# Kernel tuning notes

Hardware: AMD Instinct MI355X
Metric: run time of the kernel (lower is better)

## Reference

```python
import jax, jax.numpy as jnp
import numpy as np

N = 200000      # num nodes
D = 64          # n_dims_in == n_dims_out
Q = 4096        # num queries
G = 64          # edges per query in last step (contiguous groups, G > max_edges)
E = Q * G       # last-step edges
E0 = 131072     # earlier-step edges
K = 10          # max_edges (top-k per query)
RATIO = 0.0     # ratio_update


def setup_inputs() -> dict:
    key = jax.random.key(0)
    ks = jax.random.split(key, 14)
    # last-step edges: [E,8]; col0=query id (sorted, contiguous groups of G), col6=src, col7=dst
    q1 = jnp.repeat(jnp.arange(Q, dtype=jnp.int32), G)
    src1 = jax.random.randint(ks[0], (E,), 0, N, dtype=jnp.int32)
    dst1 = jax.random.randint(ks[1], (E,), 0, N, dtype=jnp.int32)
    edges1 = jnp.concatenate([q1[:, None], jnp.zeros((E, 5), jnp.int32), src1[:, None], dst1[:, None]], axis=1)
    # earlier-step edges: [E0,8]
    q0 = jax.random.randint(ks[2], (E0,), 0, Q, dtype=jnp.int32)
    src0 = jax.random.randint(ks[3], (E0,), 0, N, dtype=jnp.int32)
    dst0 = jax.random.randint(ks[4], (E0,), 0, N, dtype=jnp.int32)
    edges0 = jnp.concatenate([q0[:, None], jnp.zeros((E0, 5), jnp.int32), src0[:, None], dst0[:, None]], axis=1)
    std_g3 = np.float32(np.sqrt(2.0 / (4 * D)))
    std_x = np.float32(np.sqrt(2.0 / (D + D)))  # xavier_normal for linear_between_steps
    return {
        "visited_node_score": jax.random.uniform(ks[5], (N,), dtype=jnp.float32),
        "node_repr": jax.random.normal(ks[6], (N, D), dtype=jnp.float32),
        "rel_emb0": jax.random.normal(ks[7], (E0, D), dtype=jnp.float32),
        "rel_emb1": jax.random.normal(ks[8], (E, D), dtype=jnp.float32),
        "rule_prior": jax.random.normal(ks[9], (E,), dtype=jnp.float32),
        "query_src_ts_emb": jax.random.normal(ks[10], (Q, D), dtype=jnp.float32),
        "query_rel_emb": jax.random.normal(ks[11], (Q, D), dtype=jnp.float32),
        "Wq": jax.random.normal(ks[12], (4 * D, 4 * D), dtype=jnp.float32) * std_g3,
        "Wk": jax.random.normal(ks[13], (4 * D, 4 * D), dtype=jnp.float32) * std_g3,
        "W_lin": jax.random.normal(jax.random.fold_in(key, 77), (D, D), dtype=jnp.float32) * std_x,
        "b_lin": jnp.zeros((D,), dtype=jnp.float32),
        "rule_gamma": jnp.float32(1.0),
        "edges0": edges0,
        "edges1": edges1,
        "max_edges": K,
    }


def _segment_softmax(logits, seg, n):
    m = jax.ops.segment_max(logits, seg, num_segments=n)
    e = jnp.exp(logits - m[seg])
    s = jax.ops.segment_sum(e, seg, num_segments=n)
    return e / s[seg]


def _att_score(q_idx, h_vi, h_vj, rel, qst_tab, qr_tab, Wq, Wk):
    qst = qst_tab[q_idx]
    qr = qr_tab[q_idx]
    left = jnp.concatenate([h_vi, rel, qst, qr], axis=-1)   # [E, 4D]
    right = jnp.concatenate([h_vj, rel, qst, qr], axis=-1)  # [E, 4D]
    return jnp.sum((left @ Wq.T) * (right @ Wk.T), axis=-1)  # [E]


def _update_repr(src, dst, repr_, trans, n):
    # sparse mm: row src <- (1-ratio)*trans * repr[dst]; diag = 1 for non-src nodes, ratio for src nodes
    agg = jax.ops.segment_sum(trans[:, None] * repr_[dst], src, num_segments=n)
    has_src = jax.ops.segment_sum(jnp.ones_like(trans), src, num_segments=n) > 0
    diag = jnp.where(has_src, jnp.float32(RATIO), jnp.float32(1.0))
    return (1.0 - RATIO) * agg + diag[:, None] * repr_


def reference(visited_node_score, node_repr, rel_emb0, rel_emb1, rule_prior,
              query_src_ts_emb, query_rel_emb, Wq, Wk, W_lin, b_lin, rule_gamma,
              edges0, edges1, max_edges):
    n = node_repr.shape[0]
    qid, src, dst = edges1[:, 0], edges1[:, 6], edges1[:, 7]
    # last propagation step: rule-aware attention
    logits = _att_score(qid, node_repr[src], node_repr[dst], rel_emb1,
                        query_src_ts_emb, query_rel_emb, Wq, Wk) + rule_gamma * rule_prior
    src_score = visited_node_score[src]
    trans = _segment_softmax(logits, src, n)
    target_score = trans * src_score
    # per-query top-k (groups are contiguous blocks of size G, all > k)
    ts2 = target_score.reshape(-1, G)                                 # [Q, G]
    _, idx = jax.lax.top_k(ts2, max_edges)                            # [Q, k]
    orig_indices = (jnp.arange(ts2.shape[0], dtype=idx.dtype)[:, None] * G + idx).reshape(-1)
    pruned_edges = edges1[orig_indices]
    trans_p = trans[orig_indices]
    pruned_src_score = src_score[orig_indices]
    # node score update: sparse [n, Ep] @ src_score == scatter-add by target node (col 7)
    updated_node_score = jax.ops.segment_sum(trans_p * pruned_src_score, pruned_edges[:, 7], num_segments=n)
    updated_repr = _update_repr(pruned_edges[:, 6], pruned_edges[:, 7], node_repr, trans_p, n)
    # earlier step (back-propagation of representations)
    s0, d0 = edges0[:, 6], edges0[:, 7]
    l0 = _att_score(edges0[:, 0], updated_repr[s0], updated_repr[d0], rel_emb0,
                    query_src_ts_emb, query_rel_emb, Wq, Wk)
    t0 = _segment_softmax(l0, s0, n)
    updated_repr = _update_repr(s0, d0, updated_repr, t0, n)
    # bypass_forward: LeakyReLU(Linear(.))
    updated_repr = jax.nn.leaky_relu(updated_repr @ W_lin.T + b_lin, negative_slope=0.01)
    return updated_node_score, updated_repr, pruned_edges, orig_indices
```

## Files before the change

### kernel.cpp

```cpp
#include <hip/hip_runtime.h>

#define NN 200000
#define QQ 4096
#define GG 64
#define EE 262144
#define EE0 131072
#define KK 10
#define QKp (QQ*KK)

#define o_M      0
#define o_GpT    16384
#define o_P      65536
#define o_sQ     1114112
#define o_segmax 1118208
#define o_segsum 1318208
#define o_has    1518208
#define o_elog   1718208
#define o_rm22   1980352
#define o_target 2242496
#define o_psrc   2504640
#define o_pdst   2545600
#define o_pt     2586560
#define o_g      2627520
#define o_end    (o_g+12800000)

__device__ __forceinline__ float dot4(float4 a, float4 b){
  return a.x*b.x + a.y*b.y + a.z*b.z + a.w*b.w;
}
__device__ __forceinline__ unsigned fenc(float f){
  unsigned u = __float_as_uint(f);
  return (u & 0x80000000u) ? ~u : (u | 0x80000000u);
}
__device__ __forceinline__ float fdec(unsigned e){
  return (e & 0x80000000u) ? __uint_as_float(e ^ 0x80000000u) : __uint_as_float(~e);
}

__global__ void computeG_k(const float* __restrict__ Wq, const float* __restrict__ Wk,
                           float* __restrict__ G){
  __shared__ float wa[64][64], wb[64][64];
  int m = blockIdx.x;
  int aoff = (m>>2)*64, boff = (m&3)*64;
  int t = threadIdx.x;
  int j = t & 63, g = t >> 6;
  float acc[16];
  #pragma unroll
  for (int ii=0; ii<16; ii++) acc[ii]=0.f;
  for (int k0=0; k0<256; k0+=64){
    for (int s=0; s<16; s++){
      int kk = g*16 + s;
      wa[kk][j] = Wq[(k0+kk)*256 + aoff + j];
      wb[kk][j] = Wk[(k0+kk)*256 + boff + j];
    }
    __syncthreads();
    for (int kk=0; kk<64; kk++){
      float bv = wb[kk][j];
      #pragma unroll
      for (int ii=0; ii<16; ii++) acc[ii] += wa[kk][g*16+ii]*bv;
    }
    __syncthreads();
  }
  for (int ii=0; ii<16; ii++) G[(aoff + g*16+ii)*256 + boff + j] = acc[ii];
}

__global__ void repack_k(const float* __restrict__ G, float* __restrict__ M,
                         float* __restrict__ GpT){
  int t = blockIdx.x*256 + threadIdx.x;
  if (t < 16384){
    int m = t >> 12, r = (t >> 6) & 63, c = t & 63;
    float v;
    if (m==0)      v = G[r*256 + c];
    else if (m==1) v = G[(64+r)*256 + c];
    else if (m==2) v = G[c*256 + 64 + r];
    else           v = G[(64+r)*256 + 64 + c];
    M[t] = v;
  } else {
    int u = t - 16384;
    int j = u / 384, i = u - j*384;
    GpT[u] = (i < 128) ? G[i*256 + 128 + j] : G[(128+j)*256 + (i-128)];
  }
}

__global__ void pq_k(const float* __restrict__ QST, const float* __restrict__ QR,
                     const float* __restrict__ GpT, float* __restrict__ P,
                     float* __restrict__ sQ){
  __shared__ float xs[4][128];
  int wv = threadIdx.x >> 6, lane = threadIdx.x & 63;
  int q = blockIdx.x*4 + wv;
  xs[wv][lane]      = QST[(size_t)q*64 + lane];
  xs[wv][64 + lane] = QR[(size_t)q*64 + lane];
  __syncthreads();
  float4 accP = {0.f,0.f,0.f,0.f};
  float4 accY = {0.f,0.f,0.f,0.f};
  for (int j=0; j<128; j++){
    float xv = xs[wv][j];
    float4 gpv = ((const float4*)(GpT + j*384))[lane];
    accP.x += gpv.x*xv; accP.y += gpv.y*xv; accP.z += gpv.z*xv; accP.w += gpv.w*xv;
    if (lane < 32){
      float4 gyv = ((const float4*)(GpT + j*384 + 256))[lane];
      accY.x += gyv.x*xv; accY.y += gyv.y*xv; accY.z += gyv.z*xv; accY.w += gyv.w*xv;
    }
  }
  ((float4*)(P + (size_t)q*256))[lane] = accP;
  float sq = 0.f;
  if (lane < 32){
    sq = accY.x*xs[wv][4*lane] + accY.y*xs[wv][4*lane+1]
       + accY.z*xs[wv][4*lane+2] + accY.w*xs[wv][4*lane+3];
  }
  #pragma unroll
  for (int off=32; off>0; off>>=1) sq += __shfl_xor(sq, off, 64);
  if (lane == 0) sQ[q] = sq;
}

__global__ void matvec64_k(const float* __restrict__ X, const float* __restrict__ W,
                           float* __restrict__ O, int rows){
  int r = blockIdx.x*blockDim.x + threadIdx.x;
  if (r >= rows) return;
  const float4* Xv = (const float4*)(X + (size_t)r*64);
  float4 x[16];
  #pragma unroll
  for (int jj=0;jj<16;jj++) x[jj] = Xv[jj];
  const float4* Wv = (const float4*)W;
  float4* Ov = (float4*)(O + (size_t)r*64);
  for (int i0=0; i0<16; i0++){
    float a[4];
    #pragma unroll
    for (int ii=0; ii<4; ii++){
      float s=0.f;
      #pragma unroll
      for (int jj=0;jj<16;jj++) s += dot4(Wv[(i0*4+ii)*16+jj], x[jj]);
      a[ii]=s;
    }
    Ov[i0] = make_float4(a[0],a[1],a[2],a[3]);
  }
}

__global__ void quadform_k(const float* __restrict__ X, const float* __restrict__ W,
                           float* __restrict__ O, int rows){
  int r = blockIdx.x*blockDim.x + threadIdx.x;
  if (r >= rows) return;
  const float4* Xv = (const float4*)(X + (size_t)r*64);
  float4 x[16];
  #pragma unroll
  for (int jj=0;jj<16;jj++) x[jj] = Xv[jj];
  const float4* Wv = (const float4*)W;
  float acc = 0.f;
  #pragma unroll
  for (int i0=0; i0<16; i0++){
    float xi[4] = {x[i0].x, x[i0].y, x[i0].z, x[i0].w};
    #pragma unroll
    for (int ii=0; ii<4; ii++){
      float s=0.f;
      #pragma unroll
      for (int jj=0;jj<16;jj++) s += dot4(Wv[(i0*4+ii)*16+jj], x[jj]);
      acc += xi[ii]*s;
    }
  }
  O[r] = acc;
}

__global__ void linear_leaky_k(const float* __restrict__ X, const float* __restrict__ W,
                               const float* __restrict__ bias, float* __restrict__ O, int rows){
  int r = blockIdx.x*blockDim.x + threadIdx.x;
  if (r >= rows) return;
  const float4* Xv = (const float4*)(X + (size_t)r*64);
  float4 x[16];
  #pragma unroll
  for (int jj=0;jj<16;jj++) x[jj] = Xv[jj];
  const float4* Wv = (const float4*)W;
  float4* Ov = (float4*)(O + (size_t)r*64);
  for (int i0=0; i0<16; i0++){
    float a[4];
    #pragma unroll
    for (int ii=0; ii<4; ii++){
      float s = bias[i0*4+ii];
      #pragma unroll
      for (int jj=0;jj<16;jj++) s += dot4(Wv[(i0*4+ii)*16+jj], x[jj]);
      a[ii] = (s >= 0.f) ? s : 0.01f*s;
    }
    Ov[i0] = make_float4(a[0],a[1],a[2],a[3]);
  }
}

__global__ void passQ_k(const int* __restrict__ edges, const float* __restrict__ H,
                        const float* __restrict__ REL, const float* __restrict__ P,
                        const float* __restrict__ sQ, const float* __restrict__ rm22,
                        const float* __restrict__ prior, const float* __restrict__ gamma_p,
                        float* __restrict__ logits, int nE){
  int w = (blockIdx.x*blockDim.x + threadIdx.x) >> 6;
  int lane = threadIdx.x & 63;
  if (w >= nE) return;
  int q = edges[(size_t)w*8 + 0];
  int s = edges[(size_t)w*8 + 6];
  int d = edges[(size_t)w*8 + 7];
  const float* Pq = P + (size_t)q*256;
  float hs = H[(size_t)s*64 + lane];
  float hd = H[(size_t)d*64 + lane];
  float rr = REL[(size_t)w*64 + lane];
  float acc = hs*Pq[lane] + hd*Pq[128+lane] + rr*(Pq[64+lane]+Pq[192+lane]);
  #pragma unroll
  for (int off=32; off>0; off>>=1) acc += __shfl_xor(acc, off, 64);
  if (lane == 0){
    float lg = acc + sQ[q] + rm22[w];
    if (prior) lg += gamma_p[0]*prior[w];
    logits[w] = lg;
  }
}

__global__ void dot_k(const int* __restrict__ edges, const float* __restrict__ H,
                      const float* __restrict__ REL, const float* __restrict__ g,
                      float* __restrict__ logits, unsigned* __restrict__ segmax,
                      int mode, int nE){
  int w = (blockIdx.x*blockDim.x + threadIdx.x) >> 6;
  int lane = threadIdx.x & 63;
  if (w >= nE) return;
  int s = edges[(size_t)w*8 + 6];
  int d = edges[(size_t)w*8 + 7];
  float a, b;
  if (mode == 0){ a = H[(size_t)s*64 + lane];   b = g[(size_t)d*64 + lane]; }
  else if (mode == 1){ a = REL[(size_t)w*64 + lane]; b = g[(size_t)d*64 + lane]; }
  else { a = REL[(size_t)w*64 + lane]; b = g[(size_t)s*64 + lane]; }
  float acc = a*b;
  #pragma unroll
  for (int off=32; off>0; off>>=1) acc += __shfl_xor(acc, off, 64);
  if (lane == 0){
    float lg = logits[w] + acc;
    logits[w] = lg;
    if (mode == 2) atomicMax(&segmax[s], fenc(lg));
  }
}

__global__ void expsum_k(const int* __restrict__ edges, float* __restrict__ elog,
                         const unsigned* __restrict__ segmax,
                         float* __restrict__ segsum, int* __restrict__ has, int nE){
  int e = blockIdx.x*blockDim.x + threadIdx.x;
  if (e >= nE) return;
  int s = edges[(size_t)e*8 + 6];
  float m = fdec(segmax[s]);
  float ev = expf(elog[e] - m);
  elog[e] = ev;
  atomicAdd(&segsum[s], ev);
  if (has) has[s] = 1;
}

__global__ void trans_k(const int* __restrict__ edges, float* __restrict__ elog,
                        const float* __restrict__ segsum, const float* __restrict__ vscore,
                        float* __restrict__ target, int nE){
  int e = blockIdx.x*blockDim.x + threadIdx.x;
  if (e >= nE) return;
  int s = edges[(size_t)e*8 + 6];
  float t = elog[e] / segsum[s];
  elog[e] = t;
  if (target) target[e] = t * vscore[s];
}

__global__ void topk_k(const float* __restrict__ target, const float* __restrict__ trans,
                       const int* __restrict__ edges, const float* __restrict__ vscore,
                       float* __restrict__ out_score, float* __restrict__ out_pruned,
                       float* __restrict__ out_orig, int* __restrict__ psrc, int* __restrict__ pdst,
                       float* __restrict__ pt, int* __restrict__ has){
  int q = blockIdx.x*4 + (threadIdx.x>>6);
  int lane = threadIdx.x & 63;
  if (q >= QQ) return;
  float myv = target[(size_t)q*GG + lane];
  for (int j=0;j<KK;j++){
    float v = myv; int idx = lane;
    #pragma unroll
    for (int off=32; off>0; off>>=1){
      float ov = __shfl_xor(v, off, 64);
      int oi = __shfl_xor(idx, off, 64);
      if (ov > v || (ov == v && oi < idx)){ v = ov; idx = oi; }
    }
    if (lane == idx){
      myv = -__builtin_inff();
      int orig = q*GG + idx;
      out_orig[q*KK + j] = (float)orig;
      int s = edges[(size_t)orig*8 + 6];
      int d = edges[(size_t)orig*8 + 7];
      #pragma unroll
      for (int c=0;c<8;c++) out_pruned[((size_t)q*KK+j)*8 + c] = (float)edges[(size_t)orig*8 + c];
      float t = trans[orig];
      float ss = vscore[s];
      atomicAdd(&out_score[d], t*ss);
      psrc[q*KK+j] = s; pdst[q*KK+j] = d; pt[q*KK+j] = t;
      has[s] = 1;
    }
  }
}

__global__ void scatter_pruned_k(const int* __restrict__ psrc, const int* __restrict__ pdst,
                                 const float* __restrict__ pt, const float* __restrict__ H,
                                 float* __restrict__ agg){
  int p = (blockIdx.x*blockDim.x + threadIdx.x) >> 6;
  int lane = threadIdx.x & 63;
  if (p >= QKp) return;
  int s = psrc[p], d = pdst[p];
  float t = pt[p];
  atomicAdd(&agg[(size_t)s*64 + lane], t * H[(size_t)d*64 + lane]);
}

__global__ void scatter_edges_k(const int* __restrict__ edges, const float* __restrict__ trans,
                                const float* __restrict__ H, float* __restrict__ agg, int nE){
  int e = (blockIdx.x*blockDim.x + threadIdx.x) >> 6;
  int lane = threadIdx.x & 63;
  if (e >= nE) return;
  int s = edges[(size_t)e*8 + 6];
  int d = edges[(size_t)e*8 + 7];
  atomicAdd(&agg[(size_t)s*64 + lane], trans[e] * H[(size_t)d*64 + lane]);
}

__global__ void fixup_copy_k(const int* __restrict__ has, const float* __restrict__ src,
                             float* __restrict__ dstbuf){
  int i = blockIdx.x*blockDim.x + threadIdx.x;
  if (i >= NN*64) return;
  int v = i >> 6;
  if (!has[v]) dstbuf[i] = src[i];
}

extern "C" void kernel_launch(void* const* d_in, const int* in_sizes, int n_in,
                              void* d_out, int out_size, void* d_ws, size_t ws_size,
                              hipStream_t stream){
  const float* vscore    = (const float*)d_in[0];
  const float* node_repr = (const float*)d_in[1];
  const float* rel0      = (const float*)d_in[2];
  const float* rel1      = (const float*)d_in[3];
  const float* prior     = (const float*)d_in[4];
  const float* qst       = (const float*)d_in[5];
  const float* qre       = (const float*)d_in[6];
  const float* Wq        = (const float*)d_in[7];
  const float* Wk        = (const float*)d_in[8];
  const float* Wlin      = (const float*)d_in[9];
  const float* blin      = (const float*)d_in[10];
  const float* gamma     = (const float*)d_in[11];
  const int*   edges0    = (const int*)d_in[12];
  const int*   edges1    = (const int*)d_in[13];

  float* ws = (float*)d_ws;
  float* M      = ws + o_M;
  float* GpT    = ws + o_GpT;
  float* P      = ws + o_P;
  float* sQv    = ws + o_sQ;
  unsigned* segmax = (unsigned*)(ws + o_segmax);
  float* segsum = ws + o_segsum;
  int*   has    = (int*)(ws + o_has);
  float* elog   = ws + o_elog;
  float* rm22   = ws + o_rm22;
  float* target = ws + o_target;
  int*   psrc   = (int*)(ws + o_psrc);
  int*   pdst   = (int*)(ws + o_pdst);
  float* pt     = ws + o_pt;
  float* gbuf   = ws + o_g;

  float* out_score  = (float*)d_out;
  float* out_repr   = out_score + NN;
  float* out_pruned = out_repr + (size_t)NN*64;
  float* out_orig   = out_pruned + (size_t)QKp*8;

  const float* M00  = M + 0;
  const float* M10  = M + 4096;
  const float* M01T = M + 8192;
  const float* M11b = M + 12288;

  hipMemsetAsync(ws + o_segmax, 0, (size_t)600000*4, stream);
  hipMemsetAsync(out_score, 0, (size_t)(NN + (size_t)NN*64)*4, stream);

  computeG_k<<<16,256,0,stream>>>(Wq, Wk, gbuf);
  repack_k<<<256,256,0,stream>>>(gbuf, M, GpT);
  pq_k<<<QQ/4,256,0,stream>>>(qst, qre, GpT, P, sQv);

  quadform_k<<<EE/256,256,0,stream>>>(rel1, M11b, rm22, EE);
  passQ_k<<<EE/4,256,0,stream>>>(edges1, node_repr, rel1, P, sQv, rm22,
                                 prior, gamma, elog, EE);
  matvec64_k<<<(NN+255)/256,256,0,stream>>>(node_repr, M00, gbuf, NN);
  dot_k<<<EE/4,256,0,stream>>>(edges1, node_repr, rel1, gbuf, elog, segmax, 0, EE);
  matvec64_k<<<(NN+255)/256,256,0,stream>>>(node_repr, M10, gbuf, NN);
  dot_k<<<EE/4,256,0,stream>>>(edges1, node_repr, rel1, gbuf, elog, segmax, 1, EE);
  matvec64_k<<<(NN+255)/256,256,0,stream>>>(node_repr, M01T, gbuf, NN);
  dot_k<<<EE/4,256,0,stream>>>(edges1, node_repr, rel1, gbuf, elog, segmax, 2, EE);
  expsum_k<<<EE/256,256,0,stream>>>(edges1, elog, segmax, segsum, nullptr, EE);
  trans_k<<<EE/256,256,0,stream>>>(edges1, elog, segsum, vscore, target, EE);
  topk_k<<<QQ/4,256,0,stream>>>(target, elog, edges1, vscore, out_score, out_pruned, out_orig,
                                psrc, pdst, pt, has);
  scatter_pruned_k<<<(QKp*64)/256,256,0,stream>>>(psrc, pdst, pt, node_repr, out_repr);
  fixup_copy_k<<<(NN*64+255)/256,256,0,stream>>>(has, node_repr, out_repr);

  hipMemsetAsync(ws + o_segmax, 0, (size_t)600000*4, stream);
  quadform_k<<<EE0/256,256,0,stream>>>(rel0, M11b, rm22, EE0);
  passQ_k<<<EE0/4,256,0,stream>>>(edges0, out_repr, rel0, P, sQv, rm22,
                                  nullptr, nullptr, elog, EE0);
  matvec64_k<<<(NN+255)/256,256,0,stream>>>(out_repr, M00, gbuf, NN);
  dot_k<<<EE0/4,256,0,stream>>>(edges0, out_repr, rel0, gbuf, elog, segmax, 0, EE0);
  matvec64_k<<<(NN+255)/256,256,0,stream>>>(out_repr, M10, gbuf, NN);
  dot_k<<<EE0/4,256,0,stream>>>(edges0, out_repr, rel0, gbuf, elog, segmax, 1, EE0);
  matvec64_k<<<(NN+255)/256,256,0,stream>>>(out_repr, M01T, gbuf, NN);
  dot_k<<<EE0/4,256,0,stream>>>(edges0, out_repr, rel0, gbuf, elog, segmax, 2, EE0);
  expsum_k<<<EE0/256,256,0,stream>>>(edges0, elog, segmax, segsum, has, EE0);
  trans_k<<<EE0/256,256,0,stream>>>(edges0, elog, segsum, vscore, nullptr, EE0);
  hipMemsetAsync(gbuf, 0, (size_t)NN*64*4, stream);
  scatter_edges_k<<<(EE0*64)/256,256,0,stream>>>(edges0, elog, out_repr, gbuf, EE0);
  fixup_copy_k<<<(NN*64+255)/256,256,0,stream>>>(has, out_repr, gbuf);
  linear_leaky_k<<<(NN+255)/256,256,0,stream>>>(gbuf, Wlin, blin, out_repr, NN);
}
```

Baseline: 1.413 ms.

## Stage row tiles through LDS for coalesced matvec I/O and fuse init with fixup copy

The per-row matvec, quadform and linear_leaky kernels now stage 64-row tiles through padded LDS, so global loads and stores are coalesced float4 accesses instead of each thread streaming its own 256-byte row. They run as 64-thread blocks. The large memset plus fixup copy around each scatter is replaced by one init kernel that writes zeros for rows with incoming edges and copies the source for the rest, saving a full pass over the N×64 buffer. Small blocks may lower occupancy, and the launches now assume row counts divisible by 64.

```diff
diff --git a/kernel.cpp b/kernel.cpp
--- a/kernel.cpp
+++ b/kernel.cpp
@@ -7,6 +7,7 @@
 #define EE0 131072
 #define KK 10
 #define QKp (QQ*KK)
+#define PITCH 68
 
 #define o_M      0
 #define o_GpT    16384
@@ -111,16 +112,25 @@
   if (lane == 0) sQ[q] = sq;
 }
 
-__global__ void matvec64_k(const float* __restrict__ X, const float* __restrict__ W,
-                           float* __restrict__ O, int rows){
-  int r = blockIdx.x*blockDim.x + threadIdx.x;
-  if (r >= rows) return;
-  const float4* Xv = (const float4*)(X + (size_t)r*64);
+__global__ __launch_bounds__(64) void matvec64_k(const float* __restrict__ X,
+                                                 const float* __restrict__ W,
+                                                 float* __restrict__ O){
+  __shared__ float lds[64*PITCH];
+  int lane = threadIdx.x;
+  size_t base = (size_t)blockIdx.x * 64;
+  const float4* Xg = (const float4*)(X + base*64);
+  #pragma unroll
+  for (int i=0;i<16;i++){
+    int f = i*64 + lane;
+    float4 v = Xg[f];
+    *(float4*)(lds + (f>>4)*PITCH + (f&15)*4) = v;
+  }
+  __builtin_amdgcn_sched_barrier(0);
   float4 x[16];
   #pragma unroll
-  for (int jj=0;jj<16;jj++) x[jj] = Xv[jj];
+  for (int jj=0;jj<16;jj++) x[jj] = *(const float4*)(lds + lane*PITCH + jj*4);
+  __builtin_amdgcn_sched_barrier(0);
   const float4* Wv = (const float4*)W;
-  float4* Ov = (float4*)(O + (size_t)r*64);
   for (int i0=0; i0<16; i0++){
     float a[4];
     #pragma unroll
@@ -130,18 +140,34 @@
       for (int jj=0;jj<16;jj++) s += dot4(Wv[(i0*4+ii)*16+jj], x[jj]);
       a[ii]=s;
     }
-    Ov[i0] = make_float4(a[0],a[1],a[2],a[3]);
-  }
-}
-
-__global__ void quadform_k(const float* __restrict__ X, const float* __restrict__ W,
-                           float* __restrict__ O, int rows){
-  int r = blockIdx.x*blockDim.x + threadIdx.x;
-  if (r >= rows) return;
-  const float4* Xv = (const float4*)(X + (size_t)r*64);
+    *(float4*)(lds + lane*PITCH + i0*4) = make_float4(a[0],a[1],a[2],a[3]);
+  }
+  __builtin_amdgcn_sched_barrier(0);
+  float4* Og = (float4*)(O + base*64);
+  #pragma unroll
+  for (int i=0;i<16;i++){
+    int f = i*64 + lane;
+    Og[f] = *(const float4*)(lds + (f>>4)*PITCH + (f&15)*4);
+  }
+}
+
+__global__ __launch_bounds__(64) void quadform_k(const float* __restrict__ X,
+                                                 const float* __restrict__ W,
+                                                 float* __restrict__ O){
+  __shared__ float lds[64*PITCH];
+  int lane = threadIdx.x;
+  size_t base = (size_t)blockIdx.x * 64;
+  const float4* Xg = (const float4*)(X + base*64);
+  #pragma unroll
+  for (int i=0;i<16;i++){
+    int f = i*64 + lane;
+    float4 v = Xg[f];
+    *(float4*)(lds + (f>>4)*PITCH + (f&15)*4) = v;
+  }
+  __builtin_amdgcn_sched_barrier(0);
   float4 x[16];
   #pragma unroll
-  for (int jj=0;jj<16;jj++) x[jj] = Xv[jj];
+  for (int jj=0;jj<16;jj++) x[jj] = *(const float4*)(lds + lane*PITCH + jj*4);
   const float4* Wv = (const float4*)W;
   float acc = 0.f;
   #pragma unroll
@@ -155,19 +181,29 @@
       acc += xi[ii]*s;
     }
   }
-  O[r] = acc;
-}
-
-__global__ void linear_leaky_k(const float* __restrict__ X, const float* __restrict__ W,
-                               const float* __restrict__ bias, float* __restrict__ O, int rows){
-  int r = blockIdx.x*blockDim.x + threadIdx.x;
-  if (r >= rows) return;
-  const float4* Xv = (const float4*)(X + (size_t)r*64);
+  O[base + lane] = acc;
+}
+
+__global__ __launch_bounds__(64) void linear_leaky_k(const float* __restrict__ X,
+                                                     const float* __restrict__ W,
+                                                     const float* __restrict__ bias,
+                                                     float* __restrict__ O){
+  __shared__ float lds[64*PITCH];
+  int lane = threadIdx.x;
+  size_t base = (size_t)blockIdx.x * 64;
+  const float4* Xg = (const float4*)(X + base*64);
+  #pragma unroll
+  for (int i=0;i<16;i++){
+    int f = i*64 + lane;
+    float4 v = Xg[f];
+    *(float4*)(lds + (f>>4)*PITCH + (f&15)*4) = v;
+  }
+  __builtin_amdgcn_sched_barrier(0);
   float4 x[16];
   #pragma unroll
-  for (int jj=0;jj<16;jj++) x[jj] = Xv[jj];
+  for (int jj=0;jj<16;jj++) x[jj] = *(const float4*)(lds + lane*PITCH + jj*4);
+  __builtin_amdgcn_sched_barrier(0);
   const float4* Wv = (const float4*)W;
-  float4* Ov = (float4*)(O + (size_t)r*64);
   for (int i0=0; i0<16; i0++){
     float a[4];
     #pragma unroll
@@ -177,7 +213,14 @@
       for (int jj=0;jj<16;jj++) s += dot4(Wv[(i0*4+ii)*16+jj], x[jj]);
       a[ii] = (s >= 0.f) ? s : 0.01f*s;
     }
-    Ov[i0] = make_float4(a[0],a[1],a[2],a[3]);
+    *(float4*)(lds + lane*PITCH + i0*4) = make_float4(a[0],a[1],a[2],a[3]);
+  }
+  __builtin_amdgcn_sched_barrier(0);
+  float4* Og = (float4*)(O + base*64);
+  #pragma unroll
+  for (int i=0;i<16;i++){
+    int f = i*64 + lane;
+    Og[f] = *(const float4*)(lds + (f>>4)*PITCH + (f&15)*4);
   }
 }
 
@@ -287,6 +330,14 @@
   }
 }
 
+__global__ void init_upd_k(const int* __restrict__ has, const float* __restrict__ src,
+                           float* __restrict__ dst){
+  int i = blockIdx.x*256 + threadIdx.x;
+  int v = i >> 4;
+  float4 z = {0.f,0.f,0.f,0.f};
+  ((float4*)dst)[i] = has[v] ? z : ((const float4*)src)[i];
+}
+
 __global__ void scatter_pruned_k(const int* __restrict__ psrc, const int* __restrict__ pdst,
                                  const float* __restrict__ pt, const float* __restrict__ H,
                                  float* __restrict__ agg){
@@ -306,14 +357,6 @@
   int s = edges[(size_t)e*8 + 6];
   int d = edges[(size_t)e*8 + 7];
   atomicAdd(&agg[(size_t)s*64 + lane], trans[e] * H[(size_t)d*64 + lane]);
-}
-
-__global__ void fixup_copy_k(const int* __restrict__ has, const float* __restrict__ src,
-                             float* __restrict__ dstbuf){
-  int i = blockIdx.x*blockDim.x + threadIdx.x;
-  if (i >= NN*64) return;
-  int v = i >> 6;
-  if (!has[v]) dstbuf[i] = src[i];
 }
 
 extern "C" void kernel_launch(void* const* d_in, const int* in_sizes, int n_in,
@@ -361,42 +404,41 @@
   const float* M11b = M + 12288;
 
   hipMemsetAsync(ws + o_segmax, 0, (size_t)600000*4, stream);
-  hipMemsetAsync(out_score, 0, (size_t)(NN + (size_t)NN*64)*4, stream);
+  hipMemsetAsync(out_score, 0, (size_t)NN*4, stream);
 
   computeG_k<<<16,256,0,stream>>>(Wq, Wk, gbuf);
   repack_k<<<256,256,0,stream>>>(gbuf, M, GpT);
   pq_k<<<QQ/4,256,0,stream>>>(qst, qre, GpT, P, sQv);
 
-  quadform_k<<<EE/256,256,0,stream>>>(rel1, M11b, rm22, EE);
+  quadform_k<<<EE/64,64,0,stream>>>(rel1, M11b, rm22);
   passQ_k<<<EE/4,256,0,stream>>>(edges1, node_repr, rel1, P, sQv, rm22,
                                  prior, gamma, elog, EE);
-  matvec64_k<<<(NN+255)/256,256,0,stream>>>(node_repr, M00, gbuf, NN);
+  matvec64_k<<<NN/64,64,0,stream>>>(node_repr, M00, gbuf);
   dot_k<<<EE/4,256,0,stream>>>(edges1, node_repr, rel1, gbuf, elog, segmax, 0, EE);
-  matvec64_k<<<(NN+255)/256,256,0,stream>>>(node_repr, M10, gbuf, NN);
+  matvec64_k<<<NN/64,64,0,stream>>>(node_repr, M10, gbuf);
   dot_k<<<EE/4,256,0,stream>>>(edges1, node_repr, rel1, gbuf, elog, segmax, 1, EE);
-  matvec64_k<<<(NN+255)/256,256,0,stream>>>(node_repr, M01T, gbuf, NN);
+  matvec64_k<<<NN/64,64,0,stream>>>(node_repr, M01T, gbuf);
   dot_k<<<EE/4,256,0,stream>>>(edges1, node_repr, rel1, gbuf, elog, segmax, 2, EE);
   expsum_k<<<EE/256,256,0,stream>>>(edges1, elog, segmax, segsum, nullptr, EE);
   trans_k<<<EE/256,256,0,stream>>>(edges1, elog, segsum, vscore, target, EE);
   topk_k<<<QQ/4,256,0,stream>>>(target, elog, edges1, vscore, out_score, out_pruned, out_orig,
                                 psrc, pdst, pt, has);
+  init_upd_k<<<NN*16/256,256,0,stream>>>(has, node_repr, out_repr);
   scatter_pruned_k<<<(QKp*64)/256,256,0,stream>>>(psrc, pdst, pt, node_repr, out_repr);
-  fixup_copy_k<<<(NN*64+255)/256,256,0,stream>>>(has, node_repr, out_repr);
 
   hipMemsetAsync(ws + o_segmax, 0, (size_t)600000*4, stream);
-  quadform_k<<<EE0/256,256,0,stream>>>(rel0, M11b, rm22, EE0);
+  quadform_k<<<EE0/64,64,0,stream>>>(rel0, M11b, rm22);
   passQ_k<<<EE0/4,256,0,stream>>>(edges0, out_repr, rel0, P, sQv, rm22,
                                   nullptr, nullptr, elog, EE0);
-  matvec64_k<<<(NN+255)/256,256,0,stream>>>(out_repr, M00, gbuf, NN);
+  matvec64_k<<<NN/64,64,0,stream>>>(out_repr, M00, gbuf);
   dot_k<<<EE0/4,256,0,stream>>>(edges0, out_repr, rel0, gbuf, elog, segmax, 0, EE0);
-  matvec64_k<<<(NN+255)/256,256,0,stream>>>(out_repr, M10, gbuf, NN);
+  matvec64_k<<<NN/64,64,0,stream>>>(out_repr, M10, gbuf);
   dot_k<<<EE0/4,256,0,stream>>>(edges0, out_repr, rel0, gbuf, elog, segmax, 1, EE0);
-  matvec64_k<<<(NN+255)/256,256,0,stream>>>(out_repr, M01T, gbuf, NN);
+  matvec64_k<<<NN/64,64,0,stream>>>(out_repr, M01T, gbuf);
   dot_k<<<EE0/4,256,0,stream>>>(edges0, out_repr, rel0, gbuf, elog, segmax, 2, EE0);
   expsum_k<<<EE0/256,256,0,stream>>>(edges0, elog, segmax, segsum, has, EE0);
   trans_k<<<EE0/256,256,0,stream>>>(edges0, elog, segsum, vscore, nullptr, EE0);
-  hipMemsetAsync(gbuf, 0, (size_t)NN*64*4, stream);
+  init_upd_k<<<NN*16/256,256,0,stream>>>(has, out_repr, gbuf);
   scatter_edges_k<<<(EE0*64)/256,256,0,stream>>>(edges0, elog, out_repr, gbuf, EE0);
-  fixup_copy_k<<<(NN*64+255)/256,256,0,stream>>>(has, out_repr, gbuf);
-  linear_leaky_k<<<(NN+255)/256,256,0,stream>>>(gbuf, Wlin, blin, out_repr, NN);
-}
+  linear_leaky_k<<<NN/64,64,0,stream>>>(gbuf, Wlin, blin, out_repr);
+}
```

Result: faster. 1.365 ms (-3.4%).
